# Performance work log

Measured on AMD Instinct MI355X. Metric: run time of the kernel, lower is better.

Reference implementation:

```python
import jax, jax.numpy as jnp
import numpy as np

N_LAYERS = 4
N_HEADS = 16

def layer_norm(x, s, b):
    m = jnp.mean(x, axis=-1, keepdims=True)
    v = jnp.mean((x - m) ** 2, axis=-1, keepdims=True)
    return (x - m) * jax.lax.rsqrt(v + 1e-5) * s + b

def patchify(x, p):
    # x: (N, c, H, W) -> (N, p*p, c*(H//p)*(W//p)); p patches per side
    N, c, H, W = x.shape
    ph, pw = H // p, W // p
    x = x.reshape(N, c, p, ph, p, pw).transpose(0, 2, 4, 1, 3, 5)
    return x.reshape(N, p * p, c * ph * pw)

def depatchify(x, p, c, ph, pw):
    # inverse of patchify: (N, p*p, c*ph*pw) -> (N, c, p*ph, p*pw)
    N = x.shape[0]
    x = x.reshape(N, p, p, c, ph, pw).transpose(0, 3, 1, 4, 2, 5)
    return x.reshape(N, c, p * ph, p * pw)

def _layer(x, allowed, wqkv, bqkv, wo, bo, s1, sb1, w1, fb1, w2, fb2, s2, sb2):
    B, S, D = x.shape
    hd = D // N_HEADS
    h = layer_norm(x, s1, sb1)
    q, k, v = jnp.split(h @ wqkv + bqkv, 3, axis=-1)
    q = q.reshape(B, S, N_HEADS, hd)
    k = k.reshape(B, S, N_HEADS, hd)
    v = v.reshape(B, S, N_HEADS, hd)
    scores = jnp.einsum('bqhd,bkhd->bhqk', q, k) * (hd ** -0.5)
    scores = jnp.where(allowed, scores, jnp.finfo(scores.dtype).min)
    a = jax.nn.softmax(scores, axis=-1)
    o = jnp.einsum('bhqk,bkhd->bqhd', a, v).reshape(B, S, D)
    x = x + o @ wo + bo
    h = layer_norm(x, s2, sb2)
    return x + jax.nn.gelu(h @ w1 + fb1) @ w2 + fb2

def _forward(f, g, pre_W, pre_b, post_W, post_b, patch_pos, func_pos,
             Wqkv, bqkv, Wo, bo, ln1_s, ln1_b, W1, b1, W2, b2, ln2_s, ln2_b):
    bs, pairs, c, H, W = f.shape
    p2, d = patch_pos.shape
    p = int(round(p2 ** 0.5))
    ph, pw = H // p, W // p
    # interleave condition/qoi: (bs, pairs, 2, c, H, W)
    x = jnp.concatenate((f[:, :, None], g[:, :, None]), axis=2)
    feat = patchify(x.reshape(bs * pairs * 2, c, H, W), p)      # (N, p2, c*ph*pw)
    feat = feat @ pre_W + pre_b + patch_pos                      # pre_proj + patch pos enc
    feat = feat.reshape(bs, pairs * 2, p2, d) + func_pos[:pairs * 2][None, :, None, :]
    S = pairs * 2 * p2
    feat = feat.reshape(bs, S, d)
    # alternating-block lower-triangular mask (uniform block size p2 since patch_num_in == patch_num_out)
    blocks = jnp.arange(S) // p2
    allowed = blocks[None, :] <= blocks[:, None]
    for i in range(N_LAYERS):
        feat = _layer(feat, allowed, Wqkv[i], bqkv[i], Wo[i], bo[i],
                      ln1_s[i], ln1_b[i], W1[i], b1[i], W2[i], b2[i], ln2_s[i], ln2_b[i])
    feat = feat.reshape(bs, pairs, 2, p2, d)[:, :, 0]            # keep condition-token outputs
    feat = feat @ post_W + post_b                                # post_proj
    feat = depatchify(feat.reshape(bs * pairs, p2, -1), p, c, ph, pw)
    feat = feat.reshape(bs, pairs, c, H, W)
    return feat[:, :-1], feat[:, -1:]                            # (ex_pred, qn_pred)

def setup_inputs():
    key = jax.random.key(0)
    ks = jax.random.split(key, 12)
    bs, pairs, c, H, W = 1, 5, 3, 128, 128
    p, d, dff, L = 16, 1024, 4096, N_LAYERS
    pin = c * (H // p) * (W // p)  # dim_channel * patch_resolution^2 = 192
    rn = lambda k, sh, sc: jax.random.normal(k, sh, jnp.float32) * sc
    return {
        'f': rn(ks[0], (bs, pairs, c, H, W), 1.0),
        'g': rn(ks[1], (bs, pairs, c, H, W), 1.0),
        'pre_W': rn(ks[2], (pin, d), 0.05), 'pre_b': jnp.zeros((d,), jnp.float32),
        'post_W': rn(ks[3], (d, pin), 0.03), 'post_b': jnp.zeros((pin,), jnp.float32),
        'patch_pos': rn(ks[4], (p * p, d), 0.02),
        'func_pos': rn(ks[5], (2 * pairs, d), 0.02),
        'Wqkv': rn(ks[6], (L, d, 3 * d), 0.03), 'bqkv': jnp.zeros((L, 3 * d), jnp.float32),
        'Wo': rn(ks[7], (L, d, d), 0.03), 'bo': jnp.zeros((L, d), jnp.float32),
        'ln1_s': jnp.ones((L, d), jnp.float32), 'ln1_b': jnp.zeros((L, d), jnp.float32),
        'W1': rn(ks[8], (L, d, dff), 0.03), 'b1': jnp.zeros((L, dff), jnp.float32),
        'W2': rn(ks[9], (L, dff, d), 0.02), 'b2': jnp.zeros((L, d), jnp.float32),
        'ln2_s': jnp.ones((L, d), jnp.float32), 'ln2_b': jnp.zeros((L, d), jnp.float32),
    }

def reference(f, g, pre_W, pre_b, post_W, post_b, patch_pos, func_pos,
              Wqkv, bqkv, Wo, bo, ln1_s, ln1_b, W1, b1, W2, b2, ln2_s, ln2_b):
    return _forward(f, g, pre_W, pre_b, post_W, post_b, patch_pos, func_pos,
                    Wqkv, bqkv, Wo, bo, ln1_s, ln1_b, W1, b1, W2, b2, ln2_s, ln2_b)
```

## Files before the change

kernel.cpp:

```cpp
#include <hip/hip_runtime.h>
#include <hip/hip_bf16.h>
#include <math.h>

#define DMODEL 1024
#define DFF    4096
#define NTOK   2560
#define PIN    192

typedef __attribute__((ext_vector_type(8))) __bf16 bf16x8;
typedef __attribute__((ext_vector_type(4))) __bf16 bf16x4;
typedef __attribute__((ext_vector_type(4))) float  f32x4;

#define MFMA16(a, b, c) __builtin_amdgcn_mfma_f32_16x16x32_bf16(a, b, c, 0, 0, 0)

__device__ __forceinline__ float gelu_f(float x) {
    const float x3 = x * x * x;
    return 0.5f * x * (1.0f + tanhf(0.7978845608028654f * (x + 0.044715f * x3)));
}

__device__ __forceinline__ void gload16(const void* g, void* l) {
    __builtin_amdgcn_global_load_lds((const __attribute__((address_space(1))) void*)g,
                                     (__attribute__((address_space(3))) void*)l, 16, 0, 0);
}

__device__ __forceinline__ void split_bf(float v, __bf16& hi, __bf16& lo) {
    hi = (__bf16)v;
    lo = (__bf16)(v - (float)hi);
}


__global__ __launch_bounds__(256) void patch_pre_kernel(
    const float* __restrict__ f, const float* __restrict__ g,
    const float* __restrict__ preW, const float* __restrict__ preb,
    const float* __restrict__ ppos, const float* __restrict__ fpos,
    float* __restrict__ out) {
    const int s0  = blockIdx.x * 4;
    const int tid = threadIdx.x;
    const int n    = s0 >> 8;
    const int pair = n >> 1, t = n & 1;
    const float* src = t ? g : f;

    __shared__ float patch[4][PIN];
    for (int l = tid; l < 4 * PIN; l += 256) {
        const int tok = l / PIN, kk = l - tok * PIN;
        const int pidx = (s0 & 255) + tok;
        const int cc = kk >> 6, a = (kk >> 3) & 7, b = kk & 7;
        const int i = pidx >> 4, j = pidx & 15;
        patch[tok][kk] = src[((size_t)(pair * 3 + cc) * 128 + (i * 8 + a)) * 128 + (j * 8 + b)];
    }
    __syncthreads();

    const int n0 = tid * 4;
    float acc[4][4] = {};
    for (int k = 0; k < PIN; ++k) {
        const float4 w = *(const float4*)(preW + (size_t)k * DMODEL + n0);
#pragma unroll
        for (int tok = 0; tok < 4; ++tok) {
            const float pv = patch[tok][k];
            acc[tok][0] += pv * w.x; acc[tok][1] += pv * w.y;
            acc[tok][2] += pv * w.z; acc[tok][3] += pv * w.w;
        }
    }
    const float4 pb = *(const float4*)(preb + n0);
    const float4 fp = *(const float4*)(fpos + (size_t)n * DMODEL + n0);
#pragma unroll
    for (int tok = 0; tok < 4; ++tok) {
        const int pidx = (s0 & 255) + tok;
        const float4 pp = *(const float4*)(ppos + (size_t)pidx * DMODEL + n0);
        float4 o;
        o.x = acc[tok][0] + pb.x + pp.x + fp.x;
        o.y = acc[tok][1] + pb.y + pp.y + fp.y;
        o.z = acc[tok][2] + pb.z + pp.z + fp.z;
        o.w = acc[tok][3] + pb.w + pp.w + fp.w;
        *(float4*)(out + (size_t)(s0 + tok) * DMODEL + n0) = o;
    }
}

__global__ __launch_bounds__(256) void wprep_kernel(
    const float* __restrict__ W, __bf16* __restrict__ WT, int K, int N) {
    const int n0 = blockIdx.x * 32, k0 = blockIdx.y * 32;
    const int tid = threadIdx.x;
    __shared__ float t[32][33];

    {
        const int kl = tid >> 3, nq = (tid & 7) * 4;
        const float4 v = *(const float4*)(W + (size_t)(k0 + kl) * N + n0 + nq);
        t[kl][nq] = v.x; t[kl][nq + 1] = v.y; t[kl][nq + 2] = v.z; t[kl][nq + 3] = v.w;
    }
    __syncthreads();

    const int nl = tid >> 3, kq = (tid & 7) * 4;
    const int n = n0 + nl;
    bf16x4 h4, l4;
#pragma unroll
    for (int i = 0; i < 4; ++i) {
        __bf16 hi, lo;
        split_bf(t[kq + i][nl], hi, lo);
        h4[i] = hi; l4[i] = lo;
    }
    const size_t base = (size_t)n * 2 * K + (size_t)(k0 >> 5) * 64 + (kq & 7);
    const int sl = kq >> 3, key = n & 7;
    *(bf16x4*)&WT[base + (size_t)((sl ^ key) << 3)]       = h4;
    *(bf16x4*)&WT[base + (size_t)(((sl | 4) ^ key) << 3)] = l4;
}

__global__ __launch_bounds__(256) void ln_split_kernel(
    const float* __restrict__ x, const float* __restrict__ gam,
    const float* __restrict__ bet, __bf16* __restrict__ o) {
    const int row = blockIdx.x, tid = threadIdx.x;
    const float* xr = x + (size_t)row * DMODEL;
    const float4 v = *(const float4*)(xr + tid * 4);

    __shared__ float red[4];
    __shared__ float stat[2];

    float s = v.x + v.y + v.z + v.w;
#pragma unroll
    for (int off = 32; off; off >>= 1) s += __shfl_down(s, off, 64);
    if ((tid & 63) == 0) red[tid >> 6] = s;
    __syncthreads();
    if (tid == 0) stat[0] = (red[0] + red[1] + red[2] + red[3]) * (1.0f / DMODEL);
    __syncthreads();
    const float m = stat[0];
    const float dx = v.x - m, dy = v.y - m, dz = v.z - m, dw = v.w - m;
    float ss = dx * dx + dy * dy + dz * dz + dw * dw;
#pragma unroll
    for (int off = 32; off; off >>= 1) ss += __shfl_down(ss, off, 64);
    if ((tid & 63) == 0) red[tid >> 6] = ss;
    __syncthreads();
    if (tid == 0) stat[1] = rsqrtf((red[0] + red[1] + red[2] + red[3]) * (1.0f / DMODEL) + 1e-5f);
    __syncthreads();
    const float rstd = stat[1];

    const float4 gv = *(const float4*)(gam + tid * 4);
    const float4 bv = *(const float4*)(bet + tid * 4);
    float ov[4];
    ov[0] = dx * rstd * gv.x + bv.x;
    ov[1] = dy * rstd * gv.y + bv.y;
    ov[2] = dz * rstd * gv.z + bv.z;
    ov[3] = dw * rstd * gv.w + bv.w;

    bf16x4 h4, l4;
#pragma unroll
    for (int i = 0; i < 4; ++i) {
        __bf16 hi, lo;
        split_bf(ov[i], hi, lo);
        h4[i] = hi; l4[i] = lo;
    }
    const int k0 = tid * 4;
    const size_t base = (size_t)row * 2048 + (size_t)(k0 >> 5) * 64 + (k0 & 7);
    const int sl = (k0 >> 3) & 3, key = row & 7;
    *(bf16x4*)&o[base + (size_t)((sl ^ key) << 3)]       = h4;
    *(bf16x4*)&o[base + (size_t)(((sl | 4) ^ key) << 3)] = l4;
}

template <int EPI>
__global__ __launch_bounds__(256) void gemm_mfma(
    const __bf16* __restrict__ A, const __bf16* __restrict__ B,
    const float* __restrict__ bias, float* __restrict__ resout,
    __bf16* __restrict__ bfout, int M, int N, int K) {
    __shared__ __bf16 sm[2][2][128 * 64];
    const int tid = threadIdx.x;
    const int w = tid >> 6, l = tid & 63;
    const int bm = blockIdx.y, bn = blockIdx.x;
    const int mat = w >> 1, half = w & 1;

    const size_t rowBytes = (size_t)K * 4;
    const char* gsrc = (const char*)(mat ? B : A)
        + (size_t)((mat ? bn : bm) * 128 + half * 64 + (l >> 3)) * rowBytes
        + (size_t)(l & 7) * 16;

    auto STAGE = [&](int buf, int kb) {
        const char* s = gsrc + (size_t)kb * 128;
#pragma unroll
        for (int it = 0; it < 8; ++it)
            gload16(s + (size_t)(it * 8) * rowBytes,
                    (void*)&sm[buf][mat][(size_t)(half * 64 + it * 8) * 64]);
    };

    f32x4 acc[4][4];
#pragma unroll
    for (int i = 0; i < 4; ++i)
#pragma unroll
        for (int j = 0; j < 4; ++j) acc[i][j] = f32x4{0.f, 0.f, 0.f, 0.f};

    const int lr = l & 15, lk = l >> 4;
    const int wr = (w >> 1) * 64, wc = (w & 1) * 64;
    const int nk = K >> 5;

    STAGE(0, 0);
    __syncthreads();

    for (int kb = 0; kb < nk; ++kb) {
        const int buf = kb & 1;
        if (kb + 1 < nk) STAGE(buf ^ 1, kb + 1);

        const __bf16* As = sm[buf][0];
        const __bf16* Bs = sm[buf][1];
        bf16x8 ah[4], al[4], bh[4], bl[4];
#pragma unroll
        for (int i = 0; i < 4; ++i) {
            const int row = wr + i * 16 + lr, kx = row & 7;
            ah[i] = *(const bf16x8*)&As[(size_t)row * 64 + ((lk ^ kx) << 3)];
            al[i] = *(const bf16x8*)&As[(size_t)row * 64 + (((lk | 4) ^ kx) << 3)];
            const int col = wc + i * 16 + lr, ky = col & 7;
            bh[i] = *(const bf16x8*)&Bs[(size_t)col * 64 + ((lk ^ ky) << 3)];
            bl[i] = *(const bf16x8*)&Bs[(size_t)col * 64 + (((lk | 4) ^ ky) << 3)];
        }
#pragma unroll
        for (int i = 0; i < 4; ++i)
#pragma unroll
            for (int j = 0; j < 4; ++j) {
                acc[i][j] = MFMA16(ah[i], bh[j], acc[i][j]);
                acc[i][j] = MFMA16(al[i], bh[j], acc[i][j]);
                acc[i][j] = MFMA16(ah[i], bl[j], acc[i][j]);
            }
        __syncthreads();
    }

#pragma unroll
    for (int j = 0; j < 4; ++j) {
        const int col = bn * 128 + wc + j * 16 + lr;
        const float bv = bias[col];
#pragma unroll
        for (int i = 0; i < 4; ++i) {
#pragma unroll
            for (int r = 0; r < 4; ++r) {
                const int rr = bm * 128 + wr + i * 16 + lk * 4 + r;
                const float v = acc[i][j][r] + bv;
                if (EPI == 0) {
                    bfout[(size_t)rr * N + col] = (__bf16)v;
                } else if (EPI == 1) {
                    const size_t id = (size_t)rr * N + col;
                    resout[id] += v;
                } else {
                    const float gv2 = gelu_f(v);
                    __bf16 hi, lo;
                    split_bf(gv2, hi, lo);
                    const size_t base = (size_t)rr * 2 * N + (size_t)(col >> 5) * 64 + (col & 7);
                    const int sl = (col >> 3) & 3, kx = rr & 7;
                    bfout[base + (size_t)((sl ^ kx) << 3)]       = hi;
                    bfout[base + (size_t)(((sl | 4) ^ kx) << 3)] = lo;
                }
            }
        }
    }
}

__global__ __launch_bounds__(256) void attn_mfma(
    const __bf16* __restrict__ qkv, __bf16* __restrict__ o) {
    const int h  = blockIdx.x;
    const int qb = blockIdx.y;
    const int tid = threadIdx.x;
    const int w = tid >> 6, l = tid & 63;
    const int lr = l & 15, lk = l >> 4;

    __shared__ __bf16 Ks[64 * 64];
    __shared__ __bf16 Vt[64 * 64];
    __shared__ __bf16 Ps[4][16 * 64];

    const int qrow = qb * 64 + w * 16 + lr;
    const __bf16* qsrc = qkv + (size_t)qrow * 3072 + h * 64 + lk * 8;
    const bf16x8 qf0 = *(const bf16x8*)qsrc;
    const bf16x8 qf1 = *(const bf16x8*)(qsrc + 32);

    f32x4 oacc[4];
#pragma unroll
    for (int i = 0; i < 4; ++i) oacc[i] = f32x4{0.f, 0.f, 0.f, 0.f};
    float mrow[4], lrow[4];
#pragma unroll
    for (int r = 0; r < 4; ++r) { mrow[r] = -3.0e38f; lrow[r] = 0.f; }

    const int skey = tid >> 2, dc = (tid & 3) * 16;
    const int nch = ((qb >> 2) + 1) * 4;

    for (int kc = 0; kc < nch; ++kc) {
        __syncthreads();
        {
            const __bf16* kp = qkv + (size_t)(kc * 64 + skey) * 3072 + 1024 + h * 64 + dc;
            const bf16x8 k0 = *(const bf16x8*)kp;
            const bf16x8 k1 = *(const bf16x8*)(kp + 8);
            const int sl0 = dc >> 3;
            *(bf16x8*)&Ks[skey * 64 + ((sl0 ^ (skey & 7)) << 3)]       = k0;
            *(bf16x8*)&Ks[skey * 64 + (((sl0 | 1) ^ (skey & 7)) << 3)] = k1;

            const __bf16* vp = kp + 1024;
            const bf16x8 v0 = *(const bf16x8*)vp;
            const bf16x8 v1 = *(const bf16x8*)(vp + 8);
#pragma unroll
            for (int e = 0; e < 8; ++e) {
                const int d0 = dc + e, d1 = dc + 8 + e;
                Vt[d0 * 64 + (((skey >> 3) ^ (d0 & 7)) << 3) + (skey & 7)] = v0[e];
                Vt[d1 * 64 + (((skey >> 3) ^ (d1 & 7)) << 3) + (skey & 7)] = v1[e];
            }
        }
        __syncthreads();

        f32x4 sv[4];
#pragma unroll
        for (int j = 0; j < 4; ++j) {
            sv[j] = f32x4{0.f, 0.f, 0.f, 0.f};
            const int kb = j * 16 + lr, sw = kb & 7;
            const bf16x8 kb0 = *(const bf16x8*)&Ks[kb * 64 + ((lk ^ sw) << 3)];
            const bf16x8 kb1 = *(const bf16x8*)&Ks[kb * 64 + (((lk | 4) ^ sw) << 3)];
            sv[j] = MFMA16(qf0, kb0, sv[j]);
            sv[j] = MFMA16(qf1, kb1, sv[j]);
        }

#pragma unroll
        for (int r = 0; r < 4; ++r) {
            float cm = fmaxf(fmaxf(sv[0][r], sv[1][r]), fmaxf(sv[2][r], sv[3][r])) * 0.125f;
#pragma unroll
            for (int msk = 1; msk < 16; msk <<= 1) cm = fmaxf(cm, __shfl_xor(cm, msk, 64));
            const float nm = fmaxf(mrow[r], cm);
            const float sc = __expf(mrow[r] - nm);
            float rs = 0.f;
#pragma unroll
            for (int j = 0; j < 4; ++j) {
                const float p = __expf(sv[j][r] * 0.125f - nm);
                sv[j][r] = p;
                rs += p;
            }
#pragma unroll
            for (int msk = 1; msk < 16; msk <<= 1) rs += __shfl_xor(rs, msk, 64);
            lrow[r] = lrow[r] * sc + rs;
            mrow[r] = nm;
#pragma unroll
            for (int db = 0; db < 4; ++db) oacc[db][r] *= sc;
        }

#pragma unroll
        for (int j = 0; j < 4; ++j)
#pragma unroll
            for (int r = 0; r < 4; ++r) {
                const int q = lk * 4 + r, key = j * 16 + lr;
                Ps[w][q * 64 + (((key >> 3) ^ (q & 7)) << 3) + (key & 7)] = (__bf16)sv[j][r];
            }
        asm volatile("" ::: "memory");

#pragma unroll
        for (int db = 0; db < 4; ++db) {
            const int d = db * 16 + lr, dw2 = d & 7;
#pragma unroll
            for (int kk = 0; kk < 2; ++kk) {
                const int sl = kk * 4 + lk;
                const bf16x8 pa = *(const bf16x8*)&Ps[w][lr * 64 + ((sl ^ (lr & 7)) << 3)];
                const bf16x8 vb = *(const bf16x8*)&Vt[d * 64 + ((sl ^ dw2) << 3)];
                oacc[db] = MFMA16(pa, vb, oacc[db]);
            }
        }
    }

    float inv[4];
#pragma unroll
    for (int r = 0; r < 4; ++r) inv[r] = 1.0f / lrow[r];

#pragma unroll
    for (int db = 0; db < 4; ++db)
#pragma unroll
        for (int r = 0; r < 4; ++r) {
            const float v = oacc[db][r] * inv[r];
            const int rr = qb * 64 + w * 16 + lk * 4 + r;
            const int col = h * 64 + db * 16 + lr;
            __bf16 hi, lo;
            split_bf(v, hi, lo);
            const size_t base = (size_t)rr * 2048 + (size_t)(col >> 5) * 64 + (col & 7);
            const int sl = (col >> 3) & 3, kx = rr & 7;
            o[base + (size_t)((sl ^ kx) << 3)]       = hi;
            o[base + (size_t)(((sl | 4) ^ kx) << 3)] = lo;
        }
}

template <int EPI>
__global__ __launch_bounds__(256) void gemm64k(
    const float* __restrict__ A, const float* __restrict__ B,
    const float* __restrict__ bias, const float* __restrict__ res,
    float* __restrict__ C, int M, int N, int K) {
    __shared__ float As[16][64];
    __shared__ float Bs[16][64];
    const int tid = threadIdx.x;
    const int bm = blockIdx.y, bn = blockIdx.x;
    const int tx = tid & 15, ty = tid >> 4;

    float acc[4][4] = {};

    const int am = tid & 63, ka = (tid >> 6) * 4;
    const int bnn = tid & 63, kb = (tid >> 6) * 4;
    const float* Ap = A + (size_t)(bm * 64 + am) * K + ka;
    const float* Bp = B + (size_t)kb * N + bn * 64 + bnn;

    for (int kt = 0; kt < K; kt += 16) {
        const float4 a0 = *(const float4*)Ap;
        const float b0 = Bp[0];
        const float b1 = Bp[(size_t)N];
        const float b2 = Bp[(size_t)2 * N];
        const float b3 = Bp[(size_t)3 * N];
        __syncthreads();
        As[ka + 0][am] = a0.x; As[ka + 1][am] = a0.y; As[ka + 2][am] = a0.z; As[ka + 3][am] = a0.w;
        Bs[kb + 0][bnn] = b0; Bs[kb + 1][bnn] = b1; Bs[kb + 2][bnn] = b2; Bs[kb + 3][bnn] = b3;
        __syncthreads();
#pragma unroll
        for (int kk = 0; kk < 16; ++kk) {
            float a[4], b[4];
            *(float4*)&a[0] = *(const float4*)&As[kk][ty * 4];
            *(float4*)&b[0] = *(const float4*)&Bs[kk][tx * 4];
#pragma unroll
            for (int i = 0; i < 4; ++i)
#pragma unroll
                for (int j = 0; j < 4; ++j)
                    acc[i][j] += a[i] * b[j];
        }
        Ap += 16;
        Bp += (size_t)16 * N;
    }

    const int col0 = bn * 64 + tx * 4;
    const float4 bv = *(const float4*)(bias + col0);
    const float* bvp = (const float*)&bv;
#pragma unroll
    for (int i = 0; i < 4; ++i) {
        const int row = bm * 64 + ty * 4 + i;
        float o0[4];
#pragma unroll
        for (int j = 0; j < 4; ++j) o0[j] = acc[i][j] + bvp[j];
        if (EPI == 1) {
            const float4 r0 = *(const float4*)(res + (size_t)row * N + col0);
            o0[0] += r0.x; o0[1] += r0.y; o0[2] += r0.z; o0[3] += r0.w;
        }
        *(float4*)(C + (size_t)row * N + col0) = make_float4(o0[0], o0[1], o0[2], o0[3]);
    }
}

__global__ __launch_bounds__(256) void gather_f_kernel(
    const float* __restrict__ x, float* __restrict__ ftok) {
    const int r = blockIdx.x;
    const int pair = r >> 8, pidx = r & 255;
    const int srow = pair * 512 + pidx;
    const int c = threadIdx.x * 4;
    *(float4*)(ftok + (size_t)r * DMODEL + c) = *(const float4*)(x + (size_t)srow * DMODEL + c);
}

__global__ __launch_bounds__(192) void depatch_kernel(
    const float* __restrict__ pbuf, float* __restrict__ out) {
    const int r = blockIdx.x;
    const int tid = threadIdx.x;
    const int pair = r >> 8, pidx = r & 255;
    const int i = pidx >> 4, j = pidx & 15;
    const int cc = tid >> 6, a = (tid >> 3) & 7, b = tid & 7;
    out[((size_t)(pair * 3 + cc) * 128 + (i * 8 + a)) * 128 + (j * 8 + b)] =
        pbuf[(size_t)r * PIN + tid];
}

extern "C" void kernel_launch(void* const* d_in, const int* in_sizes, int n_in,
                              void* d_out, int out_size, void* d_ws, size_t ws_size,
                              hipStream_t stream) {
    const float* f     = (const float*)d_in[0];
    const float* g     = (const float*)d_in[1];
    const float* preW  = (const float*)d_in[2];
    const float* preb  = (const float*)d_in[3];
    const float* postW = (const float*)d_in[4];
    const float* postb = (const float*)d_in[5];
    const float* ppos  = (const float*)d_in[6];
    const float* fpos  = (const float*)d_in[7];
    const float* Wqkv  = (const float*)d_in[8];
    const float* bqkv  = (const float*)d_in[9];
    const float* Wo    = (const float*)d_in[10];
    const float* bo    = (const float*)d_in[11];
    const float* ln1s  = (const float*)d_in[12];
    const float* ln1b  = (const float*)d_in[13];
    const float* W1    = (const float*)d_in[14];
    const float* b1w   = (const float*)d_in[15];
    const float* W2    = (const float*)d_in[16];
    const float* b2w   = (const float*)d_in[17];
    const float* ln2s  = (const float*)d_in[18];
    const float* ln2b  = (const float*)d_in[19];
    float* out = (float*)d_out;

    char* p = (char*)d_ws;
    float*  x      = (float*)p;   p += (size_t)NTOK * DMODEL * 4;
    __bf16* hbufs  = (__bf16*)p;  p += (size_t)NTOK * 2048 * 2;
    __bf16* obufs  = (__bf16*)p;  p += (size_t)NTOK * 2048 * 2;
    char*   unionA = p;           p += (size_t)NTOK * 8192 * 2;
    __bf16* wT     = (__bf16*)p;  p += (size_t)4096 * 2048 * 2;

    __bf16* qkvbf = (__bf16*)unionA;
    __bf16* acts  = (__bf16*)unionA;
    float*  ftok  = (float*)unionA;
    float*  pbuf  = (float*)(unionA + (size_t)1280 * DMODEL * 4);

    patch_pre_kernel<<<NTOK / 4, 256, 0, stream>>>(f, g, preW, preb, ppos, fpos, x);

    for (int L = 0; L < 4; ++L) {
        ln_split_kernel<<<NTOK, 256, 0, stream>>>(x, ln1s + L * DMODEL, ln1b + L * DMODEL, hbufs);
        wprep_kernel<<<dim3(3072 / 32, 1024 / 32), 256, 0, stream>>>(
            Wqkv + (size_t)L * 1024 * 3072, wT, 1024, 3072);
        gemm_mfma<0><<<dim3(24, 20), 256, 0, stream>>>(
            hbufs, wT, bqkv + (size_t)L * 3072, nullptr, qkvbf, NTOK, 3072, 1024);
        attn_mfma<<<dim3(16, 40), 256, 0, stream>>>(qkvbf, obufs);
        wprep_kernel<<<dim3(1024 / 32, 1024 / 32), 256, 0, stream>>>(
            Wo + (size_t)L * 1024 * 1024, wT, 1024, 1024);
        gemm_mfma<1><<<dim3(8, 20), 256, 0, stream>>>(
            obufs, wT, bo + (size_t)L * DMODEL, x, nullptr, NTOK, 1024, 1024);
        ln_split_kernel<<<NTOK, 256, 0, stream>>>(x, ln2s + L * DMODEL, ln2b + L * DMODEL, hbufs);
        wprep_kernel<<<dim3(4096 / 32, 1024 / 32), 256, 0, stream>>>(
            W1 + (size_t)L * 1024 * 4096, wT, 1024, 4096);
        gemm_mfma<2><<<dim3(32, 20), 256, 0, stream>>>(
            hbufs, wT, b1w + (size_t)L * DFF, nullptr, acts, NTOK, 4096, 1024);
        wprep_kernel<<<dim3(1024 / 32, 4096 / 32), 256, 0, stream>>>(
            W2 + (size_t)L * 4096 * 1024, wT, 4096, 1024);
        gemm_mfma<1><<<dim3(8, 20), 256, 0, stream>>>(
            acts, wT, b2w + (size_t)L * DMODEL, x, nullptr, NTOK, 1024, 4096);
    }

    gather_f_kernel<<<1280, 256, 0, stream>>>(x, ftok);
    gemm64k<0><<<dim3(PIN / 64, 1280 / 64), 256, 0, stream>>>(
        ftok, postW, postb, nullptr, pbuf, 1280, PIN, 1024);
    depatch_kernel<<<1280, 192, 0, stream>>>(pbuf, out);
}
```

Baseline: 1.866 ms.

## Split-K the N=1024 GEMMs, remap workgroups for XCD locality

Runs the Wo and W2 projections (N=1024) as split-K with two K slices, writing fp32 partials and then reducing them with bias into the residual in a separate kernel. This doubles the workgroup count from 160, which is meant to fill the CUs of the device. It also remaps block IDs in the GEMM and the attention kernel so that neighbouring tiles and heads land on the same XCD, to improve L2 reuse. The cost is extra partial-sum traffic and one more launch per projection. Partial buffers reuse the qkv/hbufs workspace.

```diff
diff --git a/kernel.cpp b/kernel.cpp
--- a/kernel.cpp
+++ b/kernel.cpp
@@ -162,16 +162,25 @@
     __shared__ __bf16 sm[2][2][128 * 64];
     const int tid = threadIdx.x;
     const int w = tid >> 6, l = tid & 63;
-    const int bm = blockIdx.y, bn = blockIdx.x;
+
+    const int nwg = gridDim.x * gridDim.y;
+    int bid = blockIdx.y * gridDim.x + blockIdx.x;
+    bid = (bid & 7) * (nwg >> 3) + (bid >> 3);
+    const int bn = bid % gridDim.x, bm = bid / gridDim.x;
+
+    const int kz = blockIdx.z;
+    const int nkTot = K >> 5;
+    const int nk  = nkTot / gridDim.z;
+    const int kb0 = kz * nk;
+
     const int mat = w >> 1, half = w & 1;
-
     const size_t rowBytes = (size_t)K * 4;
     const char* gsrc = (const char*)(mat ? B : A)
         + (size_t)((mat ? bn : bm) * 128 + half * 64 + (l >> 3)) * rowBytes
         + (size_t)(l & 7) * 16;
 
-    auto STAGE = [&](int buf, int kb) {
-        const char* s = gsrc + (size_t)kb * 128;
+    auto STAGE = [&](int buf, int kbAbs) {
+        const char* s = gsrc + (size_t)kbAbs * 128;
 #pragma unroll
         for (int it = 0; it < 8; ++it)
             gload16(s + (size_t)(it * 8) * rowBytes,
@@ -186,14 +195,13 @@
 
     const int lr = l & 15, lk = l >> 4;
     const int wr = (w >> 1) * 64, wc = (w & 1) * 64;
-    const int nk = K >> 5;
-
-    STAGE(0, 0);
+
+    STAGE(0, kb0);
     __syncthreads();
 
     for (int kb = 0; kb < nk; ++kb) {
         const int buf = kb & 1;
-        if (kb + 1 < nk) STAGE(buf ^ 1, kb + 1);
+        if (kb + 1 < nk) STAGE(buf ^ 1, kb0 + kb + 1);
 
         const __bf16* As = sm[buf][0];
         const __bf16* Bs = sm[buf][1];
@@ -221,7 +229,7 @@
 #pragma unroll
     for (int j = 0; j < 4; ++j) {
         const int col = bn * 128 + wc + j * 16 + lr;
-        const float bv = bias[col];
+        const float bv = (EPI == 3) ? 0.f : bias[col];
 #pragma unroll
         for (int i = 0; i < 4; ++i) {
 #pragma unroll
@@ -231,8 +239,9 @@
                 if (EPI == 0) {
                     bfout[(size_t)rr * N + col] = (__bf16)v;
                 } else if (EPI == 1) {
-                    const size_t id = (size_t)rr * N + col;
-                    resout[id] += v;
+                    resout[(size_t)rr * N + col] += v;
+                } else if (EPI == 3) {
+                    resout[((size_t)kz * M + rr) * N + col] = acc[i][j][r];
                 } else {
                     const float gv2 = gelu_f(v);
                     __bf16 hi, lo;
@@ -247,10 +256,27 @@
     }
 }
 
+__global__ __launch_bounds__(256) void reduce_splitk(
+    const float* __restrict__ part, const float* __restrict__ bias,
+    float* __restrict__ x, int MN, int N) {
+    const int i = (blockIdx.x * 256 + threadIdx.x) * 4;
+    if (i >= MN) return;
+    const float4 p0 = *(const float4*)(part + i);
+    const float4 p1 = *(const float4*)(part + (size_t)MN + i);
+    const float4 bv = *(const float4*)(bias + (i & (N - 1)));
+    float4 xv = *(float4*)(x + i);
+    xv.x += p0.x + p1.x + bv.x;
+    xv.y += p0.y + p1.y + bv.y;
+    xv.z += p0.z + p1.z + bv.z;
+    xv.w += p0.w + p1.w + bv.w;
+    *(float4*)(x + i) = xv;
+}
+
 __global__ __launch_bounds__(256) void attn_mfma(
     const __bf16* __restrict__ qkv, __bf16* __restrict__ o) {
-    const int h  = blockIdx.x;
-    const int qb = blockIdx.y;
+    const int lin = blockIdx.y * gridDim.x + blockIdx.x;
+    const int h  = ((lin & 7) << 1) | ((lin >> 3) & 1);
+    const int qb = lin >> 4;
     const int tid = threadIdx.x;
     const int w = tid >> 6, l = tid & 63;
     const int lr = l & 15, lk = l >> 4;
@@ -484,7 +510,9 @@
     __bf16* wT     = (__bf16*)p;  p += (size_t)4096 * 2048 * 2;
 
     __bf16* qkvbf = (__bf16*)unionA;
+    float*  partO = (float*)unionA;
     __bf16* acts  = (__bf16*)unionA;
+    float*  partM = (float*)hbufs;
     float*  ftok  = (float*)unionA;
     float*  pbuf  = (float*)(unionA + (size_t)1280 * DMODEL * 4);
 
@@ -499,8 +527,10 @@
         attn_mfma<<<dim3(16, 40), 256, 0, stream>>>(qkvbf, obufs);
         wprep_kernel<<<dim3(1024 / 32, 1024 / 32), 256, 0, stream>>>(
             Wo + (size_t)L * 1024 * 1024, wT, 1024, 1024);
-        gemm_mfma<1><<<dim3(8, 20), 256, 0, stream>>>(
-            obufs, wT, bo + (size_t)L * DMODEL, x, nullptr, NTOK, 1024, 1024);
+        gemm_mfma<3><<<dim3(8, 20, 2), 256, 0, stream>>>(
+            obufs, wT, nullptr, partO, nullptr, NTOK, 1024, 1024);
+        reduce_splitk<<<NTOK, 256, 0, stream>>>(partO, bo + (size_t)L * DMODEL, x,
+                                                NTOK * DMODEL, DMODEL);
         ln_split_kernel<<<NTOK, 256, 0, stream>>>(x, ln2s + L * DMODEL, ln2b + L * DMODEL, hbufs);
         wprep_kernel<<<dim3(4096 / 32, 1024 / 32), 256, 0, stream>>>(
             W1 + (size_t)L * 1024 * 4096, wT, 1024, 4096);
@@ -508,8 +538,10 @@
             hbufs, wT, b1w + (size_t)L * DFF, nullptr, acts, NTOK, 4096, 1024);
         wprep_kernel<<<dim3(1024 / 32, 4096 / 32), 256, 0, stream>>>(
             W2 + (size_t)L * 4096 * 1024, wT, 4096, 1024);
-        gemm_mfma<1><<<dim3(8, 20), 256, 0, stream>>>(
-            acts, wT, b2w + (size_t)L * DMODEL, x, nullptr, NTOK, 1024, 4096);
+        gemm_mfma<3><<<dim3(8, 20, 2), 256, 0, stream>>>(
+            acts, wT, nullptr, partM, nullptr, NTOK, 1024, 4096);
+        reduce_splitk<<<NTOK, 256, 0, stream>>>(partM, b2w + (size_t)L * DMODEL, x,
+                                                NTOK * DMODEL, DMODEL);
     }
 
     gather_f_kernel<<<1280, 256, 0, stream>>>(x, ftok);
```

After: 1.740 ms. 1.07x faster.
